# Performance work log

Hardware: AMD Instinct MI355X
Metric: run time of the kernel (lower is better)

Reference implementation:

```python
import jax, jax.numpy as jnp
import numpy as np

INPUT_SIZE = 100
HIDDEN_SIZE = 200
OUTPUT_SIZE = 1


def setup_inputs() -> dict:
    key = jax.random.key(0)
    k0, k1, k2, k3, k4, k5, k6 = jax.random.split(key, 7)
    s = 1.0 / np.sqrt(HIDDEN_SIZE)  # torch RNNCell/Linear init scale
    inp = jax.random.normal(k0, (128, 1024, INPUT_SIZE), dtype=jnp.float32)
    W_ih = jax.random.uniform(k1, (HIDDEN_SIZE, INPUT_SIZE), minval=-s, maxval=s)
    W_hh = jax.random.uniform(k2, (HIDDEN_SIZE, HIDDEN_SIZE), minval=-s, maxval=s)
    b_ih = jax.random.uniform(k3, (HIDDEN_SIZE,), minval=-s, maxval=s)
    b_hh = jax.random.uniform(k4, (HIDDEN_SIZE,), minval=-s, maxval=s)
    W_out = jax.random.uniform(k5, (OUTPUT_SIZE, HIDDEN_SIZE), minval=-s, maxval=s)
    b_out = jax.random.uniform(k6, (OUTPUT_SIZE,), minval=-s, maxval=s)
    return {"input": inp, "W_ih": W_ih, "W_hh": W_hh, "b_ih": b_ih,
            "b_hh": b_hh, "W_out": W_out, "b_out": b_out}


def reference(input, W_ih, W_hh, b_ih, b_hh, W_out, b_out):
    B, T, _ = input.shape
    # Precompute input projections for all timesteps in one GEMM: [B,T,H]
    x_proj = jnp.einsum('bti,hi->bth', input, W_ih) + b_ih + b_hh

    def step(h, xp_t):  # h: [B,H], xp_t: [B,H]
        h = jax.nn.relu(xp_t + h @ W_hh.T)
        o = h @ W_out.T + b_out  # identity output nonlinearity (out_nlin='linear')
        return h, (h, o)

    h0 = jnp.zeros((B, HIDDEN_SIZE), dtype=input.dtype)
    _, (hiddens, outputs) = jax.lax.scan(step, h0, jnp.swapaxes(x_proj, 0, 1))
    outputs = jnp.swapaxes(outputs, 0, 1)  # [B,T,O]
    hiddens = jnp.swapaxes(hiddens, 0, 1)  # [B,T,H] (torch returns list of [B,H])
    return (outputs, hiddens)
```

## Files before the change

### kernel.cpp

```cpp
#include <hip/hip_runtime.h>

#define BB 128
#define TT 1024
#define II 100
#define HH 200
#define MB 16
#define NTL 13
#define KST 7
#define HSTR 232

typedef _Float16 half8  __attribute__((ext_vector_type(8)));
typedef _Float16 half4v __attribute__((ext_vector_type(4)));
typedef float    f32x4  __attribute__((ext_vector_type(4)));

__global__ __launch_bounds__(256, 1) void rnn_xproj(
    const float* __restrict__ x, const float* __restrict__ Wih,
    const float* __restrict__ bih, const float* __restrict__ bhh,
    float* __restrict__ hid)
{
    __shared__ __align__(16) float xs[128 * II];
    const int tid = threadIdx.x;
    const int j = tid;
    const int jl = (j < HH) ? j : (HH - 1);

    float4 w[25];
    const float4* wrow = (const float4*)(Wih + jl * II);
#pragma unroll
    for (int kk = 0; kk < 25; ++kk) w[kk] = wrow[kk];
    const float bias = bih[jl] + bhh[jl];

    const long long r0 = (long long)blockIdx.x * 128;
    const float4* src = (const float4*)(x + r0 * II);
    float4* dst = (float4*)xs;
    for (int p = tid; p < 128 * II / 4; p += 256) dst[p] = src[p];
    __syncthreads();

    for (int row = 0; row < 128; ++row) {
        float a0 = 0.f, a1 = 0.f, a2 = 0.f, a3 = 0.f;
        const float4* xr = (const float4*)(xs + row * II);
#pragma unroll
        for (int kk = 0; kk < 25; ++kk) {
            float4 v = xr[kk];
            a0 += w[kk].x * v.x; a1 += w[kk].y * v.y;
            a2 += w[kk].z * v.z; a3 += w[kk].w * v.w;
        }
        if (j < HH)
            hid[(r0 + row) * HH + j] = bias + ((a0 + a1) + (a2 + a3));
    }
}

__global__ __launch_bounds__(256, 1) __attribute__((amdgpu_waves_per_eu(1, 1)))
void rnn_recur(const float* __restrict__ Whh, float* __restrict__ hid)
{
    __shared__ _Float16 hl[2][MB][HSTR];

    const int tid = threadIdx.x;
    const int wv  = tid >> 6;
    const int l   = tid & 63;
    const int m   = l & 15;
    const int kq  = l >> 4;

    half8 wf[4][KST];
#pragma unroll
    for (int i = 0; i < 4; ++i) {
        const int nt = 4 * i + wv;
        const bool v = (nt < NTL);
        int j = 16 * nt + m; if (j > HH - 1) j = HH - 1;
#pragma unroll
        for (int ks = 0; ks < KST; ++ks) {
            const int k0 = 32 * ks + 8 * kq;
            half8 f;
#pragma unroll
            for (int e = 0; e < 8; ++e) f[e] = (_Float16)0.f;
            if (v && k0 < HH) {
                const float4 lo = *(const float4*)(Whh + j * HH + k0);
                const float4 hi = *(const float4*)(Whh + j * HH + k0 + 4);
                f[0] = (_Float16)lo.x; f[1] = (_Float16)lo.y;
                f[2] = (_Float16)lo.z; f[3] = (_Float16)lo.w;
                f[4] = (_Float16)hi.x; f[5] = (_Float16)hi.y;
                f[6] = (_Float16)hi.z; f[7] = (_Float16)hi.w;
            }
            wf[i][ks] = f;
        }
    }

    int  j0a[4]; bool stv[4];
#pragma unroll
    for (int i = 0; i < 4; ++i) {
        const int nt = 4 * i + wv;
        j0a[i] = 16 * nt + 4 * kq;
        stv[i] = (nt < NTL) && (j0a[i] < HH);
    }

    {
        int* zp = (int*)hl;
        for (int p = tid; p < (int)(sizeof(hl) / 4); p += 256) zp[p] = 0;
    }
    __syncthreads();

    const long long TTHH = (long long)TT * HH;
    float* mybase = hid + (long long)blockIdx.x * MB * TTHH + (long long)m * TTHH;

    float4 xpv[4];
#pragma unroll
    for (int i = 0; i < 4; ++i)
        xpv[i] = stv[i] ? *(const float4*)(mybase + j0a[i])
                        : make_float4(0.f, 0.f, 0.f, 0.f);

    int cur = 0;
#pragma unroll 1
    for (int t = 0; t < TT; ++t) {
        float4 xpn[4];
        const bool pf = (t + 1 < TT);
#pragma unroll
        for (int i = 0; i < 4; ++i)
            xpn[i] = (pf && stv[i])
                   ? *(const float4*)(mybase + (long long)(t + 1) * HH + j0a[i])
                   : make_float4(0.f, 0.f, 0.f, 0.f);

        half8 bf[KST];
        const _Float16* hb = &hl[cur][m][0];
#pragma unroll
        for (int ks = 0; ks < KST; ++ks)
            bf[ks] = *(const half8*)(hb + 32 * ks + 8 * kq);

        f32x4 acc[4];
#pragma unroll
        for (int i = 0; i < 4; ++i) acc[i] = (f32x4){0.f, 0.f, 0.f, 0.f};
#pragma unroll
        for (int ks = 0; ks < KST; ++ks) {
#pragma unroll
            for (int i = 0; i < 4; ++i)
                acc[i] = __builtin_amdgcn_mfma_f32_16x16x32_f16(
                    wf[i][ks], bf[ks], acc[i], 0, 0, 0);
        }

#pragma unroll
        for (int i = 0; i < 4; ++i) {
            if (!stv[i]) continue;
            const float h0 = fmaxf(acc[i][0] + xpv[i].x, 0.f);
            const float h1 = fmaxf(acc[i][1] + xpv[i].y, 0.f);
            const float h2 = fmaxf(acc[i][2] + xpv[i].z, 0.f);
            const float h3 = fmaxf(acc[i][3] + xpv[i].w, 0.f);
            *(float4*)(mybase + (long long)t * HH + j0a[i]) =
                make_float4(h0, h1, h2, h3);
            half4v pk = {(_Float16)h0, (_Float16)h1, (_Float16)h2, (_Float16)h3};
            *(half4v*)&hl[cur ^ 1][m][j0a[i]] = pk;
        }

        __syncthreads();
        cur ^= 1;
#pragma unroll
        for (int i = 0; i < 4; ++i) xpv[i] = xpn[i];
    }
}

__global__ __launch_bounds__(256) void rnn_out(
    const float* __restrict__ hid, const float* __restrict__ Wout,
    const float* __restrict__ bout, float* __restrict__ out)
{
    const int wave = threadIdx.x >> 6;
    const int lane = threadIdx.x & 63;

    float wv[4];
#pragma unroll
    for (int mi = 0; mi < 4; ++mi) {
        int idx = lane + 64 * mi;
        wv[mi] = (idx < HH) ? Wout[idx] : 0.f;
    }
    const float bo = bout[0];

    const long long rbase = (long long)blockIdx.x * 64;
#pragma unroll 1
    for (int rr = wave; rr < 64; rr += 4) {
        const float* hr = hid + (rbase + rr) * HH;
        float p = 0.f;
#pragma unroll
        for (int mi = 0; mi < 4; ++mi) {
            int idx = lane + 64 * mi;
            if (idx < HH) p += wv[mi] * hr[idx];
        }
#pragma unroll
        for (int off = 32; off; off >>= 1) p += __shfl_down(p, off, 64);
        if (lane == 0) out[rbase + rr] = p + bo;
    }
}

extern "C" void kernel_launch(void* const* d_in, const int* in_sizes, int n_in,
                              void* d_out, int out_size, void* d_ws, size_t ws_size,
                              hipStream_t stream)
{
    const float* x    = (const float*)d_in[0];
    const float* Wih  = (const float*)d_in[1];
    const float* Whh  = (const float*)d_in[2];
    const float* bih  = (const float*)d_in[3];
    const float* bhh  = (const float*)d_in[4];
    const float* Wout = (const float*)d_in[5];
    const float* bout = (const float*)d_in[6];

    float* out = (float*)d_out;
    float* hid = out + (long long)BB * TT;

    rnn_xproj<<<(BB * TT) / 128, 256, 0, stream>>>(x, Wih, bih, bhh, hid);
    rnn_recur<<<BB / MB, 256, 0, stream>>>(Whh, hid);
    rnn_out<<<(BB * TT) / 64, 256, 0, stream>>>(hid, Wout, bout, out);
}
```

Measured before the change: 1.181 ms.

## Deepen x-projection prefetch and defer hidden-state stores in RNN recurrence

Unrolls the recurrent loop in super-steps of 8 timesteps. Input projections are prefetched 8 steps ahead into registers, and hidden-state global stores are delayed by 8 steps so memory latency is hidden behind the serial chain. The MFMA accumulation is split into even and odd k-slices to shorten the dependent accumulator chain. The cost is more register pressure. The stored hidden states are now fp16-rounded values rather than full fp32, which changes output precision.

```diff
diff --git a/kernel.cpp b/kernel.cpp
--- a/kernel.cpp
+++ b/kernel.cpp
@@ -8,6 +8,7 @@
 #define NTL 13
 #define KST 7
 #define HSTR 232
+#define SUP 8
 
 typedef _Float16 half8  __attribute__((ext_vector_type(8)));
 typedef _Float16 half4v __attribute__((ext_vector_type(4)));
@@ -101,58 +102,88 @@
     const long long TTHH = (long long)TT * HH;
     float* mybase = hid + (long long)blockIdx.x * MB * TTHH + (long long)m * TTHH;
 
-    float4 xpv[4];
-#pragma unroll
-    for (int i = 0; i < 4; ++i)
-        xpv[i] = stv[i] ? *(const float4*)(mybase + j0a[i])
-                        : make_float4(0.f, 0.f, 0.f, 0.f);
+    float4 xpb[SUP][4];
+    half4v hreg[SUP][4];
+    const half4v zpk = {(_Float16)0.f, (_Float16)0.f, (_Float16)0.f, (_Float16)0.f};
+#pragma unroll
+    for (int e = 0; e < SUP; ++e)
+#pragma unroll
+        for (int i = 0; i < 4; ++i) {
+            hreg[e][i] = zpk;
+            xpb[e][i] = stv[i] ? *(const float4*)(mybase + (long long)e * HH + j0a[i])
+                               : make_float4(0.f, 0.f, 0.f, 0.f);
+        }
 
     int cur = 0;
 #pragma unroll 1
-    for (int t = 0; t < TT; ++t) {
-        float4 xpn[4];
-        const bool pf = (t + 1 < TT);
-#pragma unroll
-        for (int i = 0; i < 4; ++i)
-            xpn[i] = (pf && stv[i])
-                   ? *(const float4*)(mybase + (long long)(t + 1) * HH + j0a[i])
-                   : make_float4(0.f, 0.f, 0.f, 0.f);
-
-        half8 bf[KST];
-        const _Float16* hb = &hl[cur][m][0];
-#pragma unroll
-        for (int ks = 0; ks < KST; ++ks)
-            bf[ks] = *(const half8*)(hb + 32 * ks + 8 * kq);
-
-        f32x4 acc[4];
-#pragma unroll
-        for (int i = 0; i < 4; ++i) acc[i] = (f32x4){0.f, 0.f, 0.f, 0.f};
-#pragma unroll
-        for (int ks = 0; ks < KST; ++ks) {
-#pragma unroll
-            for (int i = 0; i < 4; ++i)
-                acc[i] = __builtin_amdgcn_mfma_f32_16x16x32_f16(
-                    wf[i][ks], bf[ks], acc[i], 0, 0, 0);
-        }
-
+    for (int ss = 0; ss < TT / SUP; ++ss) {
+        const bool notfirst = (ss > 0);
+        const bool notlast  = (ss + 1 < TT / SUP);
+#pragma unroll
+        for (int e = 0; e < SUP; ++e) {
+            const int t = ss * SUP + e;
+
+            half8 bf[KST];
+            const _Float16* hb = &hl[cur][m][0];
+#pragma unroll
+            for (int ks = 0; ks < KST; ++ks)
+                bf[ks] = *(const half8*)(hb + 32 * ks + 8 * kq);
+
+            f32x4 accE[4], accO[4];
+#pragma unroll
+            for (int i = 0; i < 4; ++i) {
+                accE[i] = (f32x4){0.f, 0.f, 0.f, 0.f};
+                accO[i] = (f32x4){0.f, 0.f, 0.f, 0.f};
+            }
+#pragma unroll
+            for (int ks = 0; ks < KST; ks += 2)
+#pragma unroll
+                for (int i = 0; i < 4; ++i)
+                    accE[i] = __builtin_amdgcn_mfma_f32_16x16x32_f16(
+                        wf[i][ks], bf[ks], accE[i], 0, 0, 0);
+#pragma unroll
+            for (int ks = 1; ks < KST; ks += 2)
+#pragma unroll
+                for (int i = 0; i < 4; ++i)
+                    accO[i] = __builtin_amdgcn_mfma_f32_16x16x32_f16(
+                        wf[i][ks], bf[ks], accO[i], 0, 0, 0);
+
+#pragma unroll
+            for (int i = 0; i < 4; ++i) {
+                if (!stv[i]) continue;
+                const float h0 = fmaxf(accE[i][0] + accO[i][0] + xpb[e][i].x, 0.f);
+                const float h1 = fmaxf(accE[i][1] + accO[i][1] + xpb[e][i].y, 0.f);
+                const float h2 = fmaxf(accE[i][2] + accO[i][2] + xpb[e][i].z, 0.f);
+                const float h3 = fmaxf(accE[i][3] + accO[i][3] + xpb[e][i].w, 0.f);
+                half4v pk = {(_Float16)h0, (_Float16)h1, (_Float16)h2, (_Float16)h3};
+                *(half4v*)&hl[cur ^ 1][m][j0a[i]] = pk;
+
+                if (notfirst) {
+                    half4v ov = hreg[e][i];
+                    *(float4*)(mybase + (long long)(t - SUP) * HH + j0a[i]) =
+                        make_float4((float)ov[0], (float)ov[1],
+                                    (float)ov[2], (float)ov[3]);
+                }
+                hreg[e][i] = pk;
+
+                if (notlast)
+                    xpb[e][i] = *(const float4*)(mybase + (long long)(t + SUP) * HH + j0a[i]);
+            }
+
+            __syncthreads();
+            cur ^= 1;
+        }
+    }
+
+#pragma unroll
+    for (int e = 0; e < SUP; ++e)
 #pragma unroll
         for (int i = 0; i < 4; ++i) {
             if (!stv[i]) continue;
-            const float h0 = fmaxf(acc[i][0] + xpv[i].x, 0.f);
-            const float h1 = fmaxf(acc[i][1] + xpv[i].y, 0.f);
-            const float h2 = fmaxf(acc[i][2] + xpv[i].z, 0.f);
-            const float h3 = fmaxf(acc[i][3] + xpv[i].w, 0.f);
-            *(float4*)(mybase + (long long)t * HH + j0a[i]) =
-                make_float4(h0, h1, h2, h3);
-            half4v pk = {(_Float16)h0, (_Float16)h1, (_Float16)h2, (_Float16)h3};
-            *(half4v*)&hl[cur ^ 1][m][j0a[i]] = pk;
-        }
-
-        __syncthreads();
-        cur ^= 1;
-#pragma unroll
-        for (int i = 0; i < 4; ++i) xpv[i] = xpn[i];
-    }
+            half4v ov = hreg[e][i];
+            *(float4*)(mybase + (long long)(TT - SUP + e) * HH + j0a[i]) =
+                make_float4((float)ov[0], (float)ov[1], (float)ov[2], (float)ov[3]);
+        }
 }
 
 __global__ __launch_bounds__(256) void rnn_out(
```

Measured after the change: 2.144 ms. +81.5%, slower.

## Run each recurrence block as a single wave to drop per-step barriers

Applied to the files above, without the earlier changes.

The recurrent kernel now uses one 64-lane wave per batch group instead of four. That wave holds all 13 W_hh N-tiles in registers and computes every hidden tile itself, so the per-timestep __syncthreads is no longer needed. MFMA accumulation is split into even and odd k-chains to shorten dependency chains. The next step's x-projection is prefetched per tile right after use, and the projection goes to a separate workspace buffer when one is available, so reads and writes no longer alias. The trade-off is a much heavier register load (about 364 VGPRs of weights) with a risk of spills, and serialising the 91 MFMAs per step on one wave.

```diff
diff --git a/kernel.cpp b/kernel.cpp
--- a/kernel.cpp
+++ b/kernel.cpp
@@ -16,7 +16,7 @@
 __global__ __launch_bounds__(256, 1) void rnn_xproj(
     const float* __restrict__ x, const float* __restrict__ Wih,
     const float* __restrict__ bih, const float* __restrict__ bhh,
-    float* __restrict__ hid)
+    float* __restrict__ xpdst)
 {
     __shared__ __align__(16) float xs[128 * II];
     const int tid = threadIdx.x;
@@ -45,27 +45,29 @@
             a2 += w[kk].z * v.z; a3 += w[kk].w * v.w;
         }
         if (j < HH)
-            hid[(r0 + row) * HH + j] = bias + ((a0 + a1) + (a2 + a3));
+            xpdst[(r0 + row) * HH + j] = bias + ((a0 + a1) + (a2 + a3));
     }
 }
 
-__global__ __launch_bounds__(256, 1) __attribute__((amdgpu_waves_per_eu(1, 1)))
-void rnn_recur(const float* __restrict__ Whh, float* __restrict__ hid)
+template <bool WS>
+__global__ __launch_bounds__(64, 1) __attribute__((amdgpu_waves_per_eu(1, 1)))
+void rnn_recur(const float* __restrict__ Whh, const float* xp, float* hid)
 {
+#if __has_builtin(__builtin_assume_separate_storage)
+    if constexpr (WS) __builtin_assume_separate_storage((void*)xp, (void*)hid);
+#endif
     __shared__ _Float16 hl[2][MB][HSTR];
 
-    const int tid = threadIdx.x;
-    const int wv  = tid >> 6;
-    const int l   = tid & 63;
-    const int m   = l & 15;
-    const int kq  = l >> 4;
+    const int l  = threadIdx.x;
+    const int m  = l & 15;
+    const int kq = l >> 4;
 
-    half8 wf[4][KST];
+    half8 wf[NTL][KST];
 #pragma unroll
-    for (int i = 0; i < 4; ++i) {
-        const int nt = 4 * i + wv;
-        const bool v = (nt < NTL);
-        int j = 16 * nt + m; if (j > HH - 1) j = HH - 1;
+    for (int nt = 0; nt < NTL; ++nt) {
+        const int j = 16 * nt + m;
+        const bool v = (j < HH);
+        const int jl = v ? j : (HH - 1);
 #pragma unroll
         for (int ks = 0; ks < KST; ++ks) {
             const int k0 = 32 * ks + 8 * kq;
@@ -73,85 +75,68 @@
 #pragma unroll
             for (int e = 0; e < 8; ++e) f[e] = (_Float16)0.f;
             if (v && k0 < HH) {
-                const float4 lo = *(const float4*)(Whh + j * HH + k0);
-                const float4 hi = *(const float4*)(Whh + j * HH + k0 + 4);
+                const float4 lo = *(const float4*)(Whh + jl * HH + k0);
+                const float4 hi = *(const float4*)(Whh + jl * HH + k0 + 4);
                 f[0] = (_Float16)lo.x; f[1] = (_Float16)lo.y;
                 f[2] = (_Float16)lo.z; f[3] = (_Float16)lo.w;
                 f[4] = (_Float16)hi.x; f[5] = (_Float16)hi.y;
                 f[6] = (_Float16)hi.z; f[7] = (_Float16)hi.w;
             }
-            wf[i][ks] = f;
+            wf[nt][ks] = f;
         }
     }
 
-    int  j0a[4]; bool stv[4];
-#pragma unroll
-    for (int i = 0; i < 4; ++i) {
-        const int nt = 4 * i + wv;
-        j0a[i] = 16 * nt + 4 * kq;
-        stv[i] = (nt < NTL) && (j0a[i] < HH);
-    }
-
-    {
-        int* zp = (int*)hl;
-        for (int p = tid; p < (int)(sizeof(hl) / 4); p += 256) zp[p] = 0;
-    }
-    __syncthreads();
+    for (int p = l; p < (int)(sizeof(hl) / 4); p += 64) ((int*)hl)[p] = 0;
 
     const long long TTHH = (long long)TT * HH;
-    float* mybase = hid + (long long)blockIdx.x * MB * TTHH + (long long)m * TTHH;
+    float*       hbase = hid + (long long)blockIdx.x * MB * TTHH + (long long)m * TTHH;
+    const float* xbase = xp  + (long long)blockIdx.x * MB * TTHH + (long long)m * TTHH;
 
-    float4 xpv[4];
+    float4 xq[NTL];
 #pragma unroll
-    for (int i = 0; i < 4; ++i)
-        xpv[i] = stv[i] ? *(const float4*)(mybase + j0a[i])
-                        : make_float4(0.f, 0.f, 0.f, 0.f);
+    for (int nt = 0; nt < NTL; ++nt) {
+        const int j0 = 16 * nt + 4 * kq;
+        xq[nt] = (j0 < HH) ? *(const float4*)(xbase + j0)
+                           : make_float4(0.f, 0.f, 0.f, 0.f);
+    }
 
     int cur = 0;
 #pragma unroll 1
     for (int t = 0; t < TT; ++t) {
-        float4 xpn[4];
-        const bool pf = (t + 1 < TT);
-#pragma unroll
-        for (int i = 0; i < 4; ++i)
-            xpn[i] = (pf && stv[i])
-                   ? *(const float4*)(mybase + (long long)(t + 1) * HH + j0a[i])
-                   : make_float4(0.f, 0.f, 0.f, 0.f);
-
         half8 bf[KST];
         const _Float16* hb = &hl[cur][m][0];
 #pragma unroll
         for (int ks = 0; ks < KST; ++ks)
             bf[ks] = *(const half8*)(hb + 32 * ks + 8 * kq);
 
-        f32x4 acc[4];
-#pragma unroll
-        for (int i = 0; i < 4; ++i) acc[i] = (f32x4){0.f, 0.f, 0.f, 0.f};
-#pragma unroll
-        for (int ks = 0; ks < KST; ++ks) {
-#pragma unroll
-            for (int i = 0; i < 4; ++i)
-                acc[i] = __builtin_amdgcn_mfma_f32_16x16x32_f16(
-                    wf[i][ks], bf[ks], acc[i], 0, 0, 0);
-        }
+        float*       hrow = hbase + (long long)t * HH;
+        const int    tn   = (t + 1 < TT) ? t + 1 : t;
+        const float* xrow = xbase + (long long)tn * HH;
 
 #pragma unroll
-        for (int i = 0; i < 4; ++i) {
-            if (!stv[i]) continue;
-            const float h0 = fmaxf(acc[i][0] + xpv[i].x, 0.f);
-            const float h1 = fmaxf(acc[i][1] + xpv[i].y, 0.f);
-            const float h2 = fmaxf(acc[i][2] + xpv[i].z, 0.f);
-            const float h3 = fmaxf(acc[i][3] + xpv[i].w, 0.f);
-            *(float4*)(mybase + (long long)t * HH + j0a[i]) =
-                make_float4(h0, h1, h2, h3);
-            half4v pk = {(_Float16)h0, (_Float16)h1, (_Float16)h2, (_Float16)h3};
-            *(half4v*)&hl[cur ^ 1][m][j0a[i]] = pk;
+        for (int nt = 0; nt < NTL; ++nt) {
+            f32x4 ae = (f32x4){0.f, 0.f, 0.f, 0.f};
+            f32x4 ao = (f32x4){0.f, 0.f, 0.f, 0.f};
+#pragma unroll
+            for (int ks = 0; ks < KST; ks += 2)
+                ae = __builtin_amdgcn_mfma_f32_16x16x32_f16(wf[nt][ks], bf[ks], ae, 0, 0, 0);
+#pragma unroll
+            for (int ks = 1; ks < KST; ks += 2)
+                ao = __builtin_amdgcn_mfma_f32_16x16x32_f16(wf[nt][ks], bf[ks], ao, 0, 0, 0);
+
+            const int j0 = 16 * nt + 4 * kq;
+            if (j0 < HH) {
+                const float h0 = fmaxf(ae[0] + ao[0] + xq[nt].x, 0.f);
+                const float h1 = fmaxf(ae[1] + ao[1] + xq[nt].y, 0.f);
+                const float h2 = fmaxf(ae[2] + ao[2] + xq[nt].z, 0.f);
+                const float h3 = fmaxf(ae[3] + ao[3] + xq[nt].w, 0.f);
+                *(float4*)(hrow + j0) = make_float4(h0, h1, h2, h3);
+                half4v pk = {(_Float16)h0, (_Float16)h1, (_Float16)h2, (_Float16)h3};
+                *(half4v*)&hl[cur ^ 1][m][j0] = pk;
+                xq[nt] = *(const float4*)(xrow + j0);
+            }
         }
-
-        __syncthreads();
         cur ^= 1;
-#pragma unroll
-        for (int i = 0; i < 4; ++i) xpv[i] = xpn[i];
     }
 }
 
@@ -201,7 +186,14 @@
     float* out = (float*)d_out;
     float* hid = out + (long long)BB * TT;
 
-    rnn_xproj<<<(BB * TT) / 128, 256, 0, stream>>>(x, Wih, bih, bhh, hid);
-    rnn_recur<<<BB / MB, 256, 0, stream>>>(Whh, hid);
+    const size_t xp_bytes = (size_t)BB * TT * HH * sizeof(float);
+    const bool use_ws = (ws_size >= xp_bytes);
+    float* xparr = use_ws ? (float*)d_ws : hid;
+
+    rnn_xproj<<<(BB * TT) / 128, 256, 0, stream>>>(x, Wih, bih, bhh, xparr);
+    if (use_ws)
+        rnn_recur<true><<<BB / MB, 64, 0, stream>>>(Whh, xparr, hid);
+    else
+        rnn_recur<false><<<BB / MB, 64, 0, stream>>>(Whh, xparr, hid);
     rnn_out<<<(BB * TT) / 64, 256, 0, stream>>>(hid, Wout, bout, out);
 }
```

Measured after the change: 4.142 ms. +250.7%, slower.
